# Kernel tuning notes

Hardware: AMD Instinct MI355X
Metric: run time of the kernel (lower is better)

The kernel has to match this reference:

```python
import jax, jax.numpy as jnp
import numpy as np

B, T, H, L = 64, 512, 768, 9


def _crf_logZ(logits, transitions, seqlen):
    # forward algorithm; state freezes at t >= seqlen (tfa semantics)
    Tn = logits.shape[1]
    alpha0 = logits[:, 0]  # [B,L]
    valid = (jnp.arange(1, Tn)[None, :] < seqlen[:, None]).T  # [T-1,B]
    xs = (jnp.swapaxes(logits[:, 1:], 0, 1), valid)

    def step(alpha, inp):
        logit_t, v = inp
        new = jax.nn.logsumexp(alpha[:, :, None] + transitions[None], axis=1) + logit_t
        return jnp.where(v[:, None], new, alpha), None

    alphaT, _ = jax.lax.scan(step, alpha0, xs)
    return jax.nn.logsumexp(alphaT, axis=1)  # [B]


def _crf_score(logits, transitions, label, seqlen):
    Tn = logits.shape[1]
    seqmask = (jnp.arange(Tn)[None, :] < seqlen[:, None]).astype(logits.dtype)  # [B,T]
    unary = jnp.take_along_axis(logits, label[..., None], axis=2)[..., 0]
    unary = jnp.sum(unary * seqmask, axis=1)
    trans = transitions[label[:, :-1], label[:, 1:]]
    trans = jnp.sum(trans * seqmask[:, 1:], axis=1)
    return unary + trans  # [B]


def _viterbi(logits, transitions, seqlen):
    Tn, Ln = logits.shape[1], logits.shape[2]
    alpha0 = logits[:, 0]
    valid = (jnp.arange(1, Tn)[None, :] < seqlen[:, None]).T  # [T-1,B]
    xs = (jnp.swapaxes(logits[:, 1:], 0, 1), valid)
    idL = jnp.arange(Ln, dtype=jnp.int32)

    def step(alpha, inp):
        logit_t, v = inp
        scores = alpha[:, :, None] + transitions[None]  # [B,L,L]
        new = jnp.max(scores, axis=1) + logit_t
        bp = jnp.argmax(scores, axis=1).astype(jnp.int32)  # [B,L]
        alpha = jnp.where(v[:, None], new, alpha)
        bp = jnp.where(v[:, None], bp, idL[None, :])  # identity bp on padded steps
        return alpha, bp

    alphaT, bps = jax.lax.scan(step, alpha0, xs)  # bps: [T-1,B,L]
    last = jnp.argmax(alphaT, axis=1).astype(jnp.int32)  # [B]

    def back(tag, bp):
        prev = jnp.take_along_axis(bp, tag[:, None], axis=1)[:, 0]
        return prev, tag

    first, rest = jax.lax.scan(back, last, bps, reverse=True)
    tags = jnp.concatenate([first[None], rest], axis=0)  # [T,B]
    return jnp.swapaxes(tags, 0, 1)  # [B,T]


def setup_inputs() -> dict:
    key = jax.random.key(0)
    k = jax.random.split(key, 6)
    x = jax.random.normal(k[0], (B, T, H), dtype=jnp.float32)
    W = jax.random.truncated_normal(k[1], -2.0, 2.0, (H, L), dtype=jnp.float32) * 0.02
    b = jnp.zeros((L,), dtype=jnp.float32)
    lim = float(np.sqrt(6.0 / (L + L)))  # glorot_uniform
    transitions = jax.random.uniform(k[2], (L, L), dtype=jnp.float32, minval=-lim, maxval=lim)
    label = jax.random.randint(k[3], (B, T), 0, L, dtype=jnp.int32)
    seqlen = jax.random.randint(k[4], (B,), 1, T + 1, dtype=jnp.int32)
    mask = jnp.arange(T)[None, :] < seqlen[:, None]
    return {"x": x, "W": W, "b": b, "transitions": transitions, "label": label, "seqlen": seqlen, "mask": mask}


def reference(x, W, b, transitions, label, seqlen, mask):
    logits = jnp.einsum('bth,hl->btl', x, W) + b  # dense_ner
    ll = _crf_score(logits, transitions, label, seqlen) - _crf_logZ(logits, transitions, seqlen)
    loss = jnp.mean(-ll)
    vit = _viterbi(logits, transitions, seqlen)
    seqmask = (jnp.arange(logits.shape[1])[None, :] < seqlen[:, None]).astype(jnp.float32)
    accuracy = jnp.sum((vit == label).astype(jnp.float32) * seqmask) / jnp.sum(seqlen.astype(jnp.float32))
    tp = jnp.sum(((label > 0) & (vit == label)).astype(jnp.float32))
    tn = jnp.sum(((label > 0) & (vit != label)).astype(jnp.float32))
    fp = jnp.sum((mask & (label == 0) & (vit > 0)).astype(jnp.float32))
    return vit, tp, tn, fp, loss, accuracy
```

## Files before the change

### kernel.cpp

```cpp
#include <hip/hip_runtime.h>
#include <stdint.h>
#include <math.h>

#define NB 64
#define BT 512
#define NH 768
#define NL 9
#define PBT 528
#define PADW 772

__device__ __forceinline__ float rlane(float v, int i) {
    return __int_as_float(__builtin_amdgcn_readlane(__float_as_int(v), i));
}

template<int CTRL, int RM>
__device__ __forceinline__ float dppadd(float v) {
    const int t = __builtin_amdgcn_update_dpp(0, __float_as_int(v), CTRL, RM, 0xf, true);
    return v + __int_as_float(t);
}

__device__ __forceinline__ float wave_sum_dpp(float v) {
    v = dppadd<0x111, 0xf>(v);
    v = dppadd<0x112, 0xf>(v);
    v = dppadd<0x114, 0xf>(v);
    v = dppadd<0x118, 0xf>(v);
    v = dppadd<0x142, 0xa>(v);
    v = dppadd<0x143, 0xc>(v);
    return rlane(v, 63);
}

__global__ __launch_bounds__(256, 2) void gemm_kernel(
    const float* __restrict__ x, const float* __restrict__ W,
    const float* __restrict__ bias, float* __restrict__ logits)
{
    __shared__ float wT[NL * PADW];

    const int tid  = threadIdx.x;
    const int lane = tid & 63;

    for (int i = tid; i < NH * NL; i += 256) {
        const int h = i / NL, l = i - h * NL;
        wT[l * PADW + h] = W[i];
    }
    __syncthreads();

    float wr[3][NL][4];
#pragma unroll
    for (int k = 0; k < 3; ++k)
#pragma unroll
        for (int l = 0; l < NL; ++l) {
            const float4 w4 = *(const float4*)&wT[l * PADW + k * 256 + lane * 4];
            wr[k][l][0] = w4.x; wr[k][l][1] = w4.y;
            wr[k][l][2] = w4.z; wr[k][l][3] = w4.w;
        }
    const float bj = bias[lane < NL ? lane : 0];

    const int gwave = (blockIdx.x * blockDim.x + tid) >> 6;
    const int nw    = (gridDim.x * blockDim.x) >> 6;
    const int nrows = NB * BT;
    int row = gwave;
    if (row >= nrows) return;

    const float4* xr = (const float4*)(x + (size_t)row * NH);
    float4 a0 = xr[lane], a1 = xr[64 + lane], a2 = xr[128 + lane];

    while (true) {
        const int nrow = row + nw;
        float4 b0, b1, b2;
        if (nrow < nrows) {
            const float4* xn = (const float4*)(x + (size_t)nrow * NH);
            b0 = xn[lane]; b1 = xn[64 + lane]; b2 = xn[128 + lane];
        }

        float acc[NL];
#pragma unroll
        for (int l = 0; l < NL; ++l) {
            float s = a0.x * wr[0][l][0];
            s = fmaf(a0.y, wr[0][l][1], s);
            s = fmaf(a0.z, wr[0][l][2], s);
            s = fmaf(a0.w, wr[0][l][3], s);
            s = fmaf(a1.x, wr[1][l][0], s);
            s = fmaf(a1.y, wr[1][l][1], s);
            s = fmaf(a1.z, wr[1][l][2], s);
            s = fmaf(a1.w, wr[1][l][3], s);
            s = fmaf(a2.x, wr[2][l][0], s);
            s = fmaf(a2.y, wr[2][l][1], s);
            s = fmaf(a2.z, wr[2][l][2], s);
            s = fmaf(a2.w, wr[2][l][3], s);
            acc[l] = s;
        }
        float sum[NL];
#pragma unroll
        for (int l = 0; l < NL; ++l) sum[l] = wave_sum_dpp(acc[l]);
        float outv = sum[0];
#pragma unroll
        for (int l = 1; l < NL; ++l) outv = (lane == l) ? sum[l] : outv;
        if (lane < NL) logits[(size_t)row * NL + lane] = outv + bj;

        row = nrow;
        if (row >= nrows) break;
        a0 = b0; a1 = b1; a2 = b2;
    }
}

__global__ __launch_bounds__(256) void crf_kernel(
    const float* __restrict__ logits, const float* __restrict__ trans,
    const int* __restrict__ label, const int* __restrict__ seqlen,
    float* __restrict__ vit_out, float* __restrict__ stats)
{
    __shared__ __align__(16) float lg_lds[PBT * NL];
    __shared__ float    val_lds[BT * NL];
    __shared__ float    trans_lds[NL * NL];
    __shared__ uint8_t  bp_lds[(BT - 1) * NL];
    __shared__ uint64_t packed_lds[BT - 1];
    __shared__ uint8_t  vit_lds[BT];
    __shared__ float    xw[4][4];

    const int b    = blockIdx.x;
    const int tid  = threadIdx.x;
    const int lane = tid & 63;
    const int wv   = tid >> 6;
    const int sl   = seqlen[b];
    const float* lg  = logits + (size_t)b * BT * NL;
    const int*   lab = label + (size_t)b * BT;

    {
        const float4* src = (const float4*)lg;
        float4* dst = (float4*)lg_lds;
        for (int idx = tid; idx < BT * NL / 4; idx += 256) dst[idx] = src[idx];
        for (int idx = BT * NL + tid; idx < PBT * NL; idx += 256) lg_lds[idx] = 0.f;
        if (tid < NL * NL) trans_lds[tid] = trans[tid];
    }
    __syncthreads();

    if (wv == 0) {
        const int j = lane < NL ? lane : 0;
        float E[NL];
#pragma unroll
        for (int i = 0; i < NL; ++i) E[i] = __expf(trans_lds[i * NL + j]) * 0.125f;
        float A = __expf(lg_lds[j]);
        int lc = 0;
        for (int tb = 1; tb < BT + 8; tb += 8) {
            float P[8];
#pragma unroll
            for (int s = 0; s < 8; ++s) P[s] = __expf(lg_lds[(tb + s) * NL + j]);
#pragma unroll
            for (int s = 0; s < 8; ++s) {
                const int t = tb + s;
                const float r0 = rlane(A, 0), r1 = rlane(A, 1), r2 = rlane(A, 2),
                            r3 = rlane(A, 3), r4 = rlane(A, 4), r5 = rlane(A, 5),
                            r6 = rlane(A, 6), r7 = rlane(A, 7), r8 = rlane(A, 8);
                float p0 = r0 * E[0]; p0 = fmaf(r1, E[1], p0); p0 = fmaf(r2, E[2], p0);
                float p1 = r3 * E[3]; p1 = fmaf(r4, E[4], p1); p1 = fmaf(r5, E[5], p1);
                float p2 = r6 * E[6]; p2 = fmaf(r7, E[7], p2); p2 = fmaf(r8, E[8], p2);
                const float An = ((p0 + p1) + p2) * P[s];
                A = (t < sl) ? An : A;
            }
            const float m = fmaxf(fmaxf(
                fmaxf(fmaxf(rlane(A, 0), rlane(A, 1)), fmaxf(rlane(A, 2), rlane(A, 3))),
                fmaxf(fmaxf(rlane(A, 4), rlane(A, 5)), fmaxf(rlane(A, 6), rlane(A, 7)))),
                rlane(A, 8));
            const int ex = (int)((__float_as_uint(m) >> 23) & 0xFFu) - 126;
            const float sc = __uint_as_float((uint32_t)(127 - ex) << 23);
            A *= sc;
            lc += ex;
        }
        const float sum = ((rlane(A, 0) + rlane(A, 1)) + (rlane(A, 2) + rlane(A, 3))) +
                          ((rlane(A, 4) + rlane(A, 5)) + (rlane(A, 6) + rlane(A, 7))) +
                          rlane(A, 8);
        const float logZ = logf(sum) +
            ((float)lc + 3.0f * (float)(sl - 1)) * 0.6931471805599453f;
        if (lane == 0) stats[b * 8 + 1] = logZ;
    } else if (wv == 1) {
        const int j = lane < NL ? lane : 0;
        float tc[NL];
#pragma unroll
        for (int i = 0; i < NL; ++i) tc[i] = trans_lds[i * NL + j];
        float v = lg_lds[j];
        if (lane < NL) val_lds[j] = v;
        for (int tb = 1; tb < BT + 8; tb += 8) {
            float lv[8];
#pragma unroll
            for (int s = 0; s < 8; ++s) lv[s] = lg_lds[(tb + s) * NL + j];
#pragma unroll
            for (int s = 0; s < 8; ++s) {
                const int t = tb + s;
                const float r0 = rlane(v, 0), r1 = rlane(v, 1), r2 = rlane(v, 2),
                            r3 = rlane(v, 3), r4 = rlane(v, 4), r5 = rlane(v, 5),
                            r6 = rlane(v, 6), r7 = rlane(v, 7), r8 = rlane(v, 8);
                const float c0 = r0 + tc[0], c1 = r1 + tc[1], c2 = r2 + tc[2],
                            c3 = r3 + tc[3], c4 = r4 + tc[4], c5 = r5 + tc[5],
                            c6 = r6 + tc[6], c7 = r7 + tc[7], c8 = r8 + tc[8];
                const float m = fmaxf(fmaxf(fmaxf(fmaxf(c0, c1), c2),
                                            fmaxf(fmaxf(c3, c4), c5)),
                                      fmaxf(fmaxf(c6, c7), c8));
                const float nv = m + lv[s];
                v = (t < sl) ? nv : v;
                if (lane < NL && t < BT) val_lds[t * NL + lane] = v;
            }
        }
        const float r0 = rlane(v, 0), r1 = rlane(v, 1), r2 = rlane(v, 2),
                    r3 = rlane(v, 3), r4 = rlane(v, 4), r5 = rlane(v, 5),
                    r6 = rlane(v, 6), r7 = rlane(v, 7), r8 = rlane(v, 8);
        const float m = fmaxf(fmaxf(fmaxf(fmaxf(r0, r1), r2),
                                    fmaxf(fmaxf(r3, r4), r5)),
                              fmaxf(fmaxf(r6, r7), r8));
        const int last = (r0 == m) ? 0 : (r1 == m) ? 1 : (r2 == m) ? 2 :
                         (r3 == m) ? 3 : (r4 == m) ? 4 : (r5 == m) ? 5 :
                         (r6 == m) ? 6 : (r7 == m) ? 7 : 8;
        if (lane == 0) vit_lds[BT - 1] = (uint8_t)last;
    } else if (wv == 2) {
        float s = 0.f;
        for (int t = lane; t < BT; t += 64) {
            const int lb = lab[t];
            if (t < sl) {
                s += lg_lds[t * NL + lb];
                if (t >= 1) s += trans_lds[lab[t - 1] * NL + lb];
            }
        }
#pragma unroll
        for (int off = 32; off >= 1; off >>= 1) s += __shfl_xor(s, off, 64);
        if (lane == 0) stats[b * 8 + 0] = s;
    }
    __syncthreads();

    for (int idx = tid; idx < (BT - 1) * NL; idx += 256) {
        const int tm1 = idx / NL;
        const int jj  = idx - tm1 * NL;
        const int t   = tm1 + 1;
        int bi;
        if (t >= sl) bi = jj;
        else {
            float best = val_lds[tm1 * NL] + trans_lds[jj];
            bi = 0;
#pragma unroll
            for (int i = 1; i < NL; ++i) {
                const float c = val_lds[tm1 * NL + i] + trans_lds[i * NL + jj];
                if (c > best) { best = c; bi = i; }
            }
        }
        bp_lds[idx] = (uint8_t)bi;
    }
    __syncthreads();

    for (int r = tid; r < BT - 1; r += 256) {
        uint64_t p = 0;
#pragma unroll
        for (int i = 0; i < NL; ++i)
            p |= (uint64_t)bp_lds[r * NL + i] << (4 * i);
        packed_lds[r] = p;
    }
    __syncthreads();

    if (tid == 0) {
        int tag = vit_lds[BT - 1];
        for (int t = BT - 2; t >= 0; --t) {
            const uint64_t row = packed_lds[t];
            tag = (int)((row >> (4 * tag)) & 15u);
            vit_lds[t] = (uint8_t)tag;
        }
    }
    __syncthreads();

    float accv = 0.f, tpv = 0.f, tnv = 0.f, fpv = 0.f;
    for (int t = tid; t < BT; t += 256) {
        const int tg = vit_lds[t];
        const int lb = lab[t];
        const bool msk = t < sl;
        vit_out[(size_t)b * BT + t] = (float)tg;
        if (msk && tg == lb) accv += 1.f;
        if (lb > 0 && tg == lb) tpv += 1.f;
        if (lb > 0 && tg != lb) tnv += 1.f;
        if (msk && lb == 0 && tg > 0) fpv += 1.f;
    }
#pragma unroll
    for (int off = 32; off >= 1; off >>= 1) {
        accv += __shfl_xor(accv, off, 64);
        tpv  += __shfl_xor(tpv,  off, 64);
        tnv  += __shfl_xor(tnv,  off, 64);
        fpv  += __shfl_xor(fpv,  off, 64);
    }
    if (lane == 0) { xw[0][wv] = accv; xw[1][wv] = tpv; xw[2][wv] = tnv; xw[3][wv] = fpv; }
    __syncthreads();
    if (tid == 0) {
        stats[b * 8 + 2] = xw[0][0] + xw[0][1] + xw[0][2] + xw[0][3];
        stats[b * 8 + 3] = xw[1][0] + xw[1][1] + xw[1][2] + xw[1][3];
        stats[b * 8 + 4] = xw[2][0] + xw[2][1] + xw[2][2] + xw[2][3];
        stats[b * 8 + 5] = xw[3][0] + xw[3][1] + xw[3][2] + xw[3][3];
    }
}

__global__ __launch_bounds__(64) void finalize_kernel(
    const float* __restrict__ stats, const int* __restrict__ seqlen,
    float* __restrict__ out)
{
    const int lane = threadIdx.x;
    float score = stats[lane * 8 + 0];
    float logZ  = stats[lane * 8 + 1];
    float accv  = stats[lane * 8 + 2];
    float tpv   = stats[lane * 8 + 3];
    float tnv   = stats[lane * 8 + 4];
    float fpv   = stats[lane * 8 + 5];
    float nll   = logZ - score;
    float slf   = (float)seqlen[lane];
#pragma unroll
    for (int off = 32; off >= 1; off >>= 1) {
        nll  += __shfl_xor(nll,  off, 64);
        accv += __shfl_xor(accv, off, 64);
        tpv  += __shfl_xor(tpv,  off, 64);
        tnv  += __shfl_xor(tnv,  off, 64);
        fpv  += __shfl_xor(fpv,  off, 64);
        slf  += __shfl_xor(slf,  off, 64);
    }
    if (lane == 0) {
        out[NB * BT + 0] = tpv;
        out[NB * BT + 1] = tnv;
        out[NB * BT + 2] = fpv;
        out[NB * BT + 3] = nll / (float)NB;
        out[NB * BT + 4] = accv / slf;
    }
}

extern "C" void kernel_launch(void* const* d_in, const int* in_sizes, int n_in,
                              void* d_out, int out_size, void* d_ws, size_t ws_size,
                              hipStream_t stream)
{
    const float* x      = (const float*)d_in[0];
    const float* W      = (const float*)d_in[1];
    const float* bias   = (const float*)d_in[2];
    const float* trans  = (const float*)d_in[3];
    const int*   label  = (const int*)d_in[4];
    const int*   seqlen = (const int*)d_in[5];

    float* out    = (float*)d_out;
    float* logits = (float*)d_ws;
    float* stats  = logits + (size_t)NB * BT * NL;

    gemm_kernel<<<512, 256, 0, stream>>>(x, W, bias, logits);
    crf_kernel<<<NB, 256, 0, stream>>>(logits, trans, label, seqlen, out, stats);
    finalize_kernel<<<1, 64, 0, stream>>>(stats, seqlen, out);
}
```

Measured before the change: 212.7 us.

## Pack four CRF sequences per wave and compute backpointers inline in Viterbi scan

The CRF kernel now handles four batch rows per block, with lanes 0-35 of one wave each owning one (sequence, label) pair. Neighbour values are gathered with ds_bpermute instead of readlane. Logits are read directly from global memory with one-block-ahead register prefetching instead of being staged in LDS. Viterbi backpointers are computed inside the forward scan, which removes the separate val_lds pass. The block count drops from 64 to 16, so the serial scans run four sequences per wave, trading the lower latency of readlane for fewer, longer-lived blocks and less total serial work.

```diff
diff --git a/kernel.cpp b/kernel.cpp
--- a/kernel.cpp
+++ b/kernel.cpp
@@ -6,11 +6,15 @@
 #define BT 512
 #define NH 768
 #define NL 9
-#define PBT 528
 #define PADW 772
+#define CBB 4
+#define BPROW 16
 
 __device__ __forceinline__ float rlane(float v, int i) {
     return __int_as_float(__builtin_amdgcn_readlane(__float_as_int(v), i));
+}
+__device__ __forceinline__ float bperm(int addr, float v) {
+    return __int_as_float(__builtin_amdgcn_ds_bpermute(addr, __float_as_int(v)));
 }
 
 template<int CTRL, int RM>
@@ -18,7 +22,6 @@
     const int t = __builtin_amdgcn_update_dpp(0, __float_as_int(v), CTRL, RM, 0xf, true);
     return v + __int_as_float(t);
 }
-
 __device__ __forceinline__ float wave_sum_dpp(float v) {
     v = dppadd<0x111, 0xf>(v);
     v = dppadd<0x112, 0xf>(v);
@@ -108,185 +111,222 @@
     const int* __restrict__ label, const int* __restrict__ seqlen,
     float* __restrict__ vit_out, float* __restrict__ stats)
 {
-    __shared__ __align__(16) float lg_lds[PBT * NL];
-    __shared__ float    val_lds[BT * NL];
     __shared__ float    trans_lds[NL * NL];
-    __shared__ uint8_t  bp_lds[(BT - 1) * NL];
-    __shared__ uint64_t packed_lds[BT - 1];
-    __shared__ uint8_t  vit_lds[BT];
+    __shared__ uint8_t  bp_lds[CBB][(BT - 1) * BPROW];
+    __shared__ uint64_t packed_lds[CBB][BT - 1];
+    __shared__ uint8_t  vit_lds[CBB][BT];
     __shared__ float    xw[4][4];
 
-    const int b    = blockIdx.x;
     const int tid  = threadIdx.x;
     const int lane = tid & 63;
     const int wv   = tid >> 6;
-    const int sl   = seqlen[b];
-    const float* lg  = logits + (size_t)b * BT * NL;
-    const int*   lab = label + (size_t)b * BT;
-
-    {
-        const float4* src = (const float4*)lg;
-        float4* dst = (float4*)lg_lds;
-        for (int idx = tid; idx < BT * NL / 4; idx += 256) dst[idx] = src[idx];
-        for (int idx = BT * NL + tid; idx < PBT * NL; idx += 256) lg_lds[idx] = 0.f;
-        if (tid < NL * NL) trans_lds[tid] = trans[tid];
-    }
-    __syncthreads();
+    const int b0   = blockIdx.x * CBB;
+
+    if (tid < NL * NL) trans_lds[tid] = trans[tid];
+    __syncthreads();
+
+    int bl = lane / 9, j = lane - bl * 9;
+    if (lane >= 36) { bl = 3; j = 8; }
+    const bool act = (lane < 36);
+    const int bg   = b0 + bl;
+    const int sl   = seqlen[bg];
+    const float* lgb = logits + (size_t)bg * BT * NL;
+    int adr[9];
+#pragma unroll
+    for (int i = 0; i < 9; ++i) adr[i] = (bl * 9 + i) * 4;
 
     if (wv == 0) {
-        const int j = lane < NL ? lane : 0;
-        float E[NL];
-#pragma unroll
-        for (int i = 0; i < NL; ++i) E[i] = __expf(trans_lds[i * NL + j]) * 0.125f;
-        float A = __expf(lg_lds[j]);
+        float E[9];
+#pragma unroll
+        for (int i = 0; i < 9; ++i) E[i] = __expf(trans_lds[i * NL + j]) * 0.125f;
+        float A = __expf(lgb[j]);
         int lc = 0;
+        float cur[8], nxt[8];
+#pragma unroll
+        for (int s = 0; s < 8; ++s) cur[s] = lgb[(1 + s) * NL + j];
         for (int tb = 1; tb < BT + 8; tb += 8) {
+#pragma unroll
+            for (int s = 0; s < 8; ++s) {
+                int tt = tb + 8 + s; tt = tt > BT - 1 ? BT - 1 : tt;
+                nxt[s] = lgb[tt * NL + j];
+            }
             float P[8];
 #pragma unroll
-            for (int s = 0; s < 8; ++s) P[s] = __expf(lg_lds[(tb + s) * NL + j]);
+            for (int s = 0; s < 8; ++s) P[s] = __expf(cur[s]);
 #pragma unroll
             for (int s = 0; s < 8; ++s) {
                 const int t = tb + s;
-                const float r0 = rlane(A, 0), r1 = rlane(A, 1), r2 = rlane(A, 2),
-                            r3 = rlane(A, 3), r4 = rlane(A, 4), r5 = rlane(A, 5),
-                            r6 = rlane(A, 6), r7 = rlane(A, 7), r8 = rlane(A, 8);
-                float p0 = r0 * E[0]; p0 = fmaf(r1, E[1], p0); p0 = fmaf(r2, E[2], p0);
-                float p1 = r3 * E[3]; p1 = fmaf(r4, E[4], p1); p1 = fmaf(r5, E[5], p1);
-                float p2 = r6 * E[6]; p2 = fmaf(r7, E[7], p2); p2 = fmaf(r8, E[8], p2);
+                const float g0 = bperm(adr[0], A), g1 = bperm(adr[1], A),
+                            g2 = bperm(adr[2], A), g3 = bperm(adr[3], A),
+                            g4 = bperm(adr[4], A), g5 = bperm(adr[5], A),
+                            g6 = bperm(adr[6], A), g7 = bperm(adr[7], A),
+                            g8 = bperm(adr[8], A);
+                float p0 = g0 * E[0]; p0 = fmaf(g1, E[1], p0); p0 = fmaf(g2, E[2], p0);
+                float p1 = g3 * E[3]; p1 = fmaf(g4, E[4], p1); p1 = fmaf(g5, E[5], p1);
+                float p2 = g6 * E[6]; p2 = fmaf(g7, E[7], p2); p2 = fmaf(g8, E[8], p2);
                 const float An = ((p0 + p1) + p2) * P[s];
                 A = (t < sl) ? An : A;
             }
-            const float m = fmaxf(fmaxf(
-                fmaxf(fmaxf(rlane(A, 0), rlane(A, 1)), fmaxf(rlane(A, 2), rlane(A, 3))),
-                fmaxf(fmaxf(rlane(A, 4), rlane(A, 5)), fmaxf(rlane(A, 6), rlane(A, 7)))),
-                rlane(A, 8));
-            const int ex = (int)((__float_as_uint(m) >> 23) & 0xFFu) - 126;
-            const float sc = __uint_as_float((uint32_t)(127 - ex) << 23);
-            A *= sc;
-            lc += ex;
-        }
-        const float sum = ((rlane(A, 0) + rlane(A, 1)) + (rlane(A, 2) + rlane(A, 3))) +
-                          ((rlane(A, 4) + rlane(A, 5)) + (rlane(A, 6) + rlane(A, 7))) +
-                          rlane(A, 8);
+            {
+                const float g0 = bperm(adr[0], A), g1 = bperm(adr[1], A),
+                            g2 = bperm(adr[2], A), g3 = bperm(adr[3], A),
+                            g4 = bperm(adr[4], A), g5 = bperm(adr[5], A),
+                            g6 = bperm(adr[6], A), g7 = bperm(adr[7], A),
+                            g8 = bperm(adr[8], A);
+                const float m = fmaxf(fmaxf(
+                    fmaxf(fmaxf(g0, g1), fmaxf(g2, g3)),
+                    fmaxf(fmaxf(g4, g5), fmaxf(g6, g7))), g8);
+                const int ex = (int)((__float_as_uint(m) >> 23) & 0xFFu) - 126;
+                const float sc = __uint_as_float((uint32_t)(127 - ex) << 23);
+                A *= sc;
+                lc += ex;
+            }
+#pragma unroll
+            for (int s = 0; s < 8; ++s) cur[s] = nxt[s];
+        }
+        const float g0 = bperm(adr[0], A), g1 = bperm(adr[1], A),
+                    g2 = bperm(adr[2], A), g3 = bperm(adr[3], A),
+                    g4 = bperm(adr[4], A), g5 = bperm(adr[5], A),
+                    g6 = bperm(adr[6], A), g7 = bperm(adr[7], A),
+                    g8 = bperm(adr[8], A);
+        const float sum = ((g0 + g1) + (g2 + g3)) + ((g4 + g5) + (g6 + g7)) + g8;
         const float logZ = logf(sum) +
             ((float)lc + 3.0f * (float)(sl - 1)) * 0.6931471805599453f;
-        if (lane == 0) stats[b * 8 + 1] = logZ;
+        if (act && j == 0) stats[bg * 8 + 1] = logZ;
     } else if (wv == 1) {
-        const int j = lane < NL ? lane : 0;
-        float tc[NL];
-#pragma unroll
-        for (int i = 0; i < NL; ++i) tc[i] = trans_lds[i * NL + j];
-        float v = lg_lds[j];
-        if (lane < NL) val_lds[j] = v;
+        float tc[9];
+#pragma unroll
+        for (int i = 0; i < 9; ++i) tc[i] = trans_lds[i * NL + j];
+        float v = lgb[j];
+        float cur[8], nxt[8];
+#pragma unroll
+        for (int s = 0; s < 8; ++s) cur[s] = lgb[(1 + s) * NL + j];
         for (int tb = 1; tb < BT + 8; tb += 8) {
-            float lv[8];
-#pragma unroll
-            for (int s = 0; s < 8; ++s) lv[s] = lg_lds[(tb + s) * NL + j];
+#pragma unroll
+            for (int s = 0; s < 8; ++s) {
+                int tt = tb + 8 + s; tt = tt > BT - 1 ? BT - 1 : tt;
+                nxt[s] = lgb[tt * NL + j];
+            }
 #pragma unroll
             for (int s = 0; s < 8; ++s) {
                 const int t = tb + s;
-                const float r0 = rlane(v, 0), r1 = rlane(v, 1), r2 = rlane(v, 2),
-                            r3 = rlane(v, 3), r4 = rlane(v, 4), r5 = rlane(v, 5),
-                            r6 = rlane(v, 6), r7 = rlane(v, 7), r8 = rlane(v, 8);
-                const float c0 = r0 + tc[0], c1 = r1 + tc[1], c2 = r2 + tc[2],
-                            c3 = r3 + tc[3], c4 = r4 + tc[4], c5 = r5 + tc[5],
-                            c6 = r6 + tc[6], c7 = r7 + tc[7], c8 = r8 + tc[8];
+                const float g0 = bperm(adr[0], v), g1 = bperm(adr[1], v),
+                            g2 = bperm(adr[2], v), g3 = bperm(adr[3], v),
+                            g4 = bperm(adr[4], v), g5 = bperm(adr[5], v),
+                            g6 = bperm(adr[6], v), g7 = bperm(adr[7], v),
+                            g8 = bperm(adr[8], v);
+                const float c0 = g0 + tc[0], c1 = g1 + tc[1], c2 = g2 + tc[2],
+                            c3 = g3 + tc[3], c4 = g4 + tc[4], c5 = g5 + tc[5],
+                            c6 = g6 + tc[6], c7 = g7 + tc[7], c8 = g8 + tc[8];
                 const float m = fmaxf(fmaxf(fmaxf(fmaxf(c0, c1), c2),
                                             fmaxf(fmaxf(c3, c4), c5)),
                                       fmaxf(fmaxf(c6, c7), c8));
-                const float nv = m + lv[s];
+                const float nv = m + cur[s];
                 v = (t < sl) ? nv : v;
-                if (lane < NL && t < BT) val_lds[t * NL + lane] = v;
-            }
-        }
-        const float r0 = rlane(v, 0), r1 = rlane(v, 1), r2 = rlane(v, 2),
-                    r3 = rlane(v, 3), r4 = rlane(v, 4), r5 = rlane(v, 5),
-                    r6 = rlane(v, 6), r7 = rlane(v, 7), r8 = rlane(v, 8);
-        const float m = fmaxf(fmaxf(fmaxf(fmaxf(r0, r1), r2),
-                                    fmaxf(fmaxf(r3, r4), r5)),
-                              fmaxf(fmaxf(r6, r7), r8));
-        const int last = (r0 == m) ? 0 : (r1 == m) ? 1 : (r2 == m) ? 2 :
-                         (r3 == m) ? 3 : (r4 == m) ? 4 : (r5 == m) ? 5 :
-                         (r6 == m) ? 6 : (r7 == m) ? 7 : 8;
-        if (lane == 0) vit_lds[BT - 1] = (uint8_t)last;
-    } else if (wv == 2) {
-        float s = 0.f;
-        for (int t = lane; t < BT; t += 64) {
+                int bi = 8;
+                bi = (c7 == m) ? 7 : bi;
+                bi = (c6 == m) ? 6 : bi;
+                bi = (c5 == m) ? 5 : bi;
+                bi = (c4 == m) ? 4 : bi;
+                bi = (c3 == m) ? 3 : bi;
+                bi = (c2 == m) ? 2 : bi;
+                bi = (c1 == m) ? 1 : bi;
+                bi = (c0 == m) ? 0 : bi;
+                bi = (t < sl) ? bi : j;
+                if (act && t < BT)
+                    bp_lds[bl][(t - 1) * BPROW + j] = (uint8_t)bi;
+            }
+#pragma unroll
+            for (int s = 0; s < 8; ++s) cur[s] = nxt[s];
+        }
+        const float g0 = bperm(adr[0], v), g1 = bperm(adr[1], v),
+                    g2 = bperm(adr[2], v), g3 = bperm(adr[3], v),
+                    g4 = bperm(adr[4], v), g5 = bperm(adr[5], v),
+                    g6 = bperm(adr[6], v), g7 = bperm(adr[7], v),
+                    g8 = bperm(adr[8], v);
+        const float m = fmaxf(fmaxf(fmaxf(fmaxf(g0, g1), g2),
+                                    fmaxf(fmaxf(g3, g4), g5)),
+                              fmaxf(fmaxf(g6, g7), g8));
+        const int last = (g0 == m) ? 0 : (g1 == m) ? 1 : (g2 == m) ? 2 :
+                         (g3 == m) ? 3 : (g4 == m) ? 4 : (g5 == m) ? 5 :
+                         (g6 == m) ? 6 : (g7 == m) ? 7 : 8;
+        if (act && j == 0) vit_lds[bl][BT - 1] = (uint8_t)last;
+    } else {
+        const int s0 = (wv - 2) * 2;
+#pragma unroll
+        for (int k = 0; k < 2; ++k) {
+            const int bb  = s0 + k;
+            const int bgs = b0 + bb;
+            const int sls = seqlen[bgs];
+            const int* lab = label + (size_t)bgs * BT;
+            const float* lgs = logits + (size_t)bgs * BT * NL;
+            float s = 0.f;
+            for (int t = lane; t < BT; t += 64) {
+                const int lb = lab[t];
+                if (t < sls) {
+                    s += lgs[t * NL + lb];
+                    if (t >= 1) s += trans_lds[lab[t - 1] * NL + lb];
+                }
+            }
+#pragma unroll
+            for (int off = 32; off >= 1; off >>= 1) s += __shfl_xor(s, off, 64);
+            if (lane == 0) stats[bgs * 8 + 0] = s;
+        }
+    }
+    __syncthreads();
+
+    for (int idx = tid; idx < CBB * (BT - 1); idx += 256) {
+        const int bb = idx / (BT - 1);
+        const int rr = idx - bb * (BT - 1);
+        uint64_t p = 0;
+#pragma unroll
+        for (int i = 0; i < NL; ++i)
+            p |= (uint64_t)bp_lds[bb][rr * BPROW + i] << (4 * i);
+        packed_lds[bb][rr] = p;
+    }
+    __syncthreads();
+
+    if (wv == 0 && lane < CBB) {
+        int tag = vit_lds[lane][BT - 1];
+        for (int t = BT - 2; t >= 0; --t) {
+            const uint64_t row = packed_lds[lane][t];
+            tag = (int)((row >> (4 * tag)) & 15u);
+            vit_lds[lane][t] = (uint8_t)tag;
+        }
+    }
+    __syncthreads();
+
+    for (int bb = 0; bb < CBB; ++bb) {
+        const int b   = b0 + bb;
+        const int sls = seqlen[b];
+        const int* lab = label + (size_t)b * BT;
+        float accv = 0.f, tpv = 0.f, tnv = 0.f, fpv = 0.f;
+        for (int t = tid; t < BT; t += 256) {
+            const int tg = vit_lds[bb][t];
             const int lb = lab[t];
-            if (t < sl) {
-                s += lg_lds[t * NL + lb];
-                if (t >= 1) s += trans_lds[lab[t - 1] * NL + lb];
-            }
-        }
-#pragma unroll
-        for (int off = 32; off >= 1; off >>= 1) s += __shfl_xor(s, off, 64);
-        if (lane == 0) stats[b * 8 + 0] = s;
-    }
-    __syncthreads();
-
-    for (int idx = tid; idx < (BT - 1) * NL; idx += 256) {
-        const int tm1 = idx / NL;
-        const int jj  = idx - tm1 * NL;
-        const int t   = tm1 + 1;
-        int bi;
-        if (t >= sl) bi = jj;
-        else {
-            float best = val_lds[tm1 * NL] + trans_lds[jj];
-            bi = 0;
-#pragma unroll
-            for (int i = 1; i < NL; ++i) {
-                const float c = val_lds[tm1 * NL + i] + trans_lds[i * NL + jj];
-                if (c > best) { best = c; bi = i; }
-            }
-        }
-        bp_lds[idx] = (uint8_t)bi;
-    }
-    __syncthreads();
-
-    for (int r = tid; r < BT - 1; r += 256) {
-        uint64_t p = 0;
-#pragma unroll
-        for (int i = 0; i < NL; ++i)
-            p |= (uint64_t)bp_lds[r * NL + i] << (4 * i);
-        packed_lds[r] = p;
-    }
-    __syncthreads();
-
-    if (tid == 0) {
-        int tag = vit_lds[BT - 1];
-        for (int t = BT - 2; t >= 0; --t) {
-            const uint64_t row = packed_lds[t];
-            tag = (int)((row >> (4 * tag)) & 15u);
-            vit_lds[t] = (uint8_t)tag;
-        }
-    }
-    __syncthreads();
-
-    float accv = 0.f, tpv = 0.f, tnv = 0.f, fpv = 0.f;
-    for (int t = tid; t < BT; t += 256) {
-        const int tg = vit_lds[t];
-        const int lb = lab[t];
-        const bool msk = t < sl;
-        vit_out[(size_t)b * BT + t] = (float)tg;
-        if (msk && tg == lb) accv += 1.f;
-        if (lb > 0 && tg == lb) tpv += 1.f;
-        if (lb > 0 && tg != lb) tnv += 1.f;
-        if (msk && lb == 0 && tg > 0) fpv += 1.f;
-    }
-#pragma unroll
-    for (int off = 32; off >= 1; off >>= 1) {
-        accv += __shfl_xor(accv, off, 64);
-        tpv  += __shfl_xor(tpv,  off, 64);
-        tnv  += __shfl_xor(tnv,  off, 64);
-        fpv  += __shfl_xor(fpv,  off, 64);
-    }
-    if (lane == 0) { xw[0][wv] = accv; xw[1][wv] = tpv; xw[2][wv] = tnv; xw[3][wv] = fpv; }
-    __syncthreads();
-    if (tid == 0) {
-        stats[b * 8 + 2] = xw[0][0] + xw[0][1] + xw[0][2] + xw[0][3];
-        stats[b * 8 + 3] = xw[1][0] + xw[1][1] + xw[1][2] + xw[1][3];
-        stats[b * 8 + 4] = xw[2][0] + xw[2][1] + xw[2][2] + xw[2][3];
-        stats[b * 8 + 5] = xw[3][0] + xw[3][1] + xw[3][2] + xw[3][3];
+            const bool msk = t < sls;
+            vit_out[(size_t)b * BT + t] = (float)tg;
+            if (msk && tg == lb) accv += 1.f;
+            if (lb > 0 && tg == lb) tpv += 1.f;
+            if (lb > 0 && tg != lb) tnv += 1.f;
+            if (msk && lb == 0 && tg > 0) fpv += 1.f;
+        }
+#pragma unroll
+        for (int off = 32; off >= 1; off >>= 1) {
+            accv += __shfl_xor(accv, off, 64);
+            tpv  += __shfl_xor(tpv,  off, 64);
+            tnv  += __shfl_xor(tnv,  off, 64);
+            fpv  += __shfl_xor(fpv,  off, 64);
+        }
+        if (lane == 0) { xw[0][wv] = accv; xw[1][wv] = tpv; xw[2][wv] = tnv; xw[3][wv] = fpv; }
+        __syncthreads();
+        if (tid == 0) {
+            stats[b * 8 + 2] = xw[0][0] + xw[0][1] + xw[0][2] + xw[0][3];
+            stats[b * 8 + 3] = xw[1][0] + xw[1][1] + xw[1][2] + xw[1][3];
+            stats[b * 8 + 4] = xw[2][0] + xw[2][1] + xw[2][2] + xw[2][3];
+            stats[b * 8 + 5] = xw[3][0] + xw[3][1] + xw[3][2] + xw[3][3];
+        }
+        __syncthreads();
     }
 }
 
@@ -337,6 +377,6 @@
     float* stats  = logits + (size_t)NB * BT * NL;
 
     gemm_kernel<<<512, 256, 0, stream>>>(x, W, bias, logits);
-    crf_kernel<<<NB, 256, 0, stream>>>(logits, trans, label, seqlen, out, stats);
+    crf_kernel<<<NB / CBB, 256, 0, stream>>>(logits, trans, label, seqlen, out, stats);
     finalize_kernel<<<1, 64, 0, stream>>>(stats, seqlen, out);
 }
```

New measurement: 273.9 us. 28.8% more time.

## Use DPP row shifts instead of readlane in CRF recurrences, fuse backpointer packing

Applied to the files above, without the earlier changes.

The forward (logZ) and Viterbi recurrences now gather neighbouring lanes' state with DPP row_shr/row_shl moves, with per-lane transition coefficients indexed by shift distance, instead of nine scalar readlane broadcasts per step. Out-of-range shifts are neutralised with zero or -1e30 coefficients. The aim is to remove the readlane-to-SGPR round trip from the serial per-timestep dependency chain. Backpointer computation is also merged with packing: each thread handles one timestep and writes the packed 64-bit row directly, which drops a byte LDS array and a barrier. The backtrace loop is unrolled. In exchange each step issues 16 DPP moves instead of 9 readlanes, and the code relies on the 9 labels sitting in lanes 0-8 of a single DPP row.

```diff
diff --git a/kernel.cpp b/kernel.cpp
--- a/kernel.cpp
+++ b/kernel.cpp
@@ -13,12 +13,17 @@
     return __int_as_float(__builtin_amdgcn_readlane(__float_as_int(v), i));
 }
 
+template<int CTRL>
+__device__ __forceinline__ float dmov(float v) {
+    return __int_as_float(__builtin_amdgcn_update_dpp(
+        0, __float_as_int(v), CTRL, 0xf, 0xf, true));
+}
+
 template<int CTRL, int RM>
 __device__ __forceinline__ float dppadd(float v) {
     const int t = __builtin_amdgcn_update_dpp(0, __float_as_int(v), CTRL, RM, 0xf, true);
     return v + __int_as_float(t);
 }
-
 __device__ __forceinline__ float wave_sum_dpp(float v) {
     v = dppadd<0x111, 0xf>(v);
     v = dppadd<0x112, 0xf>(v);
@@ -111,7 +116,6 @@
     __shared__ __align__(16) float lg_lds[PBT * NL];
     __shared__ float    val_lds[BT * NL];
     __shared__ float    trans_lds[NL * NL];
-    __shared__ uint8_t  bp_lds[(BT - 1) * NL];
     __shared__ uint64_t packed_lds[BT - 1];
     __shared__ uint8_t  vit_lds[BT];
     __shared__ float    xw[4][4];
@@ -133,11 +137,17 @@
     }
     __syncthreads();
 
+    const int j = lane < NL ? lane : 0;
+
     if (wv == 0) {
-        const int j = lane < NL ? lane : 0;
-        float E[NL];
-#pragma unroll
-        for (int i = 0; i < NL; ++i) E[i] = __expf(trans_lds[i * NL + j]) * 0.125f;
+        const float Eo = __expf(trans_lds[j * NL + j]) * 0.125f;
+        float Cs[8], Ds[8], Ms[8];
+#pragma unroll
+        for (int k = 1; k <= 8; ++k) {
+            Cs[k - 1] = (j >= k)     ? __expf(trans_lds[(j - k) * NL + j]) * 0.125f : 0.f;
+            Ds[k - 1] = (j + k <= 8) ? __expf(trans_lds[(j + k) * NL + j]) * 0.125f : 0.f;
+            Ms[k - 1] = (j + k <= 8) ? 1.f : 0.f;
+        }
         float A = __expf(lg_lds[j]);
         int lc = 0;
         for (int tb = 1; tb < BT + 8; tb += 8) {
@@ -147,35 +157,73 @@
 #pragma unroll
             for (int s = 0; s < 8; ++s) {
                 const int t = tb + s;
-                const float r0 = rlane(A, 0), r1 = rlane(A, 1), r2 = rlane(A, 2),
-                            r3 = rlane(A, 3), r4 = rlane(A, 4), r5 = rlane(A, 5),
-                            r6 = rlane(A, 6), r7 = rlane(A, 7), r8 = rlane(A, 8);
-                float p0 = r0 * E[0]; p0 = fmaf(r1, E[1], p0); p0 = fmaf(r2, E[2], p0);
-                float p1 = r3 * E[3]; p1 = fmaf(r4, E[4], p1); p1 = fmaf(r5, E[5], p1);
-                float p2 = r6 * E[6]; p2 = fmaf(r7, E[7], p2); p2 = fmaf(r8, E[8], p2);
-                const float An = ((p0 + p1) + p2) * P[s];
+                const float g1 = dmov<0x111>(A), g2 = dmov<0x112>(A),
+                            g3 = dmov<0x113>(A), g4 = dmov<0x114>(A),
+                            g5 = dmov<0x115>(A), g6 = dmov<0x116>(A),
+                            g7 = dmov<0x117>(A), g8 = dmov<0x118>(A);
+                const float h1 = dmov<0x101>(A), h2 = dmov<0x102>(A),
+                            h3 = dmov<0x103>(A), h4 = dmov<0x104>(A),
+                            h5 = dmov<0x105>(A), h6 = dmov<0x106>(A),
+                            h7 = dmov<0x107>(A), h8 = dmov<0x108>(A);
+                float s0 = A * Eo;
+                s0 = fmaf(g1, Cs[0], s0); s0 = fmaf(g2, Cs[1], s0);
+                s0 = fmaf(g3, Cs[2], s0); s0 = fmaf(g4, Cs[3], s0);
+                float s1 = g5 * Cs[4];
+                s1 = fmaf(g6, Cs[5], s1); s1 = fmaf(g7, Cs[6], s1);
+                s1 = fmaf(g8, Cs[7], s1);
+                float s2 = h1 * Ds[0];
+                s2 = fmaf(h2, Ds[1], s2); s2 = fmaf(h3, Ds[2], s2);
+                s2 = fmaf(h4, Ds[3], s2);
+                float s3 = h5 * Ds[4];
+                s3 = fmaf(h6, Ds[5], s3); s3 = fmaf(h7, Ds[6], s3);
+                s3 = fmaf(h8, Ds[7], s3);
+                const float An = ((s0 + s1) + (s2 + s3)) * P[s];
                 A = (t < sl) ? An : A;
             }
-            const float m = fmaxf(fmaxf(
-                fmaxf(fmaxf(rlane(A, 0), rlane(A, 1)), fmaxf(rlane(A, 2), rlane(A, 3))),
-                fmaxf(fmaxf(rlane(A, 4), rlane(A, 5)), fmaxf(rlane(A, 6), rlane(A, 7)))),
-                rlane(A, 8));
-            const int ex = (int)((__float_as_uint(m) >> 23) & 0xFFu) - 126;
-            const float sc = __uint_as_float((uint32_t)(127 - ex) << 23);
-            A *= sc;
-            lc += ex;
-        }
-        const float sum = ((rlane(A, 0) + rlane(A, 1)) + (rlane(A, 2) + rlane(A, 3))) +
-                          ((rlane(A, 4) + rlane(A, 5)) + (rlane(A, 6) + rlane(A, 7))) +
-                          rlane(A, 8);
-        const float logZ = logf(sum) +
-            ((float)lc + 3.0f * (float)(sl - 1)) * 0.6931471805599453f;
-        if (lane == 0) stats[b * 8 + 1] = logZ;
+            {
+                const float g1 = dmov<0x111>(A), g2 = dmov<0x112>(A),
+                            g3 = dmov<0x113>(A), g4 = dmov<0x114>(A),
+                            g5 = dmov<0x115>(A), g6 = dmov<0x116>(A),
+                            g7 = dmov<0x117>(A), g8 = dmov<0x118>(A);
+                const float h1 = dmov<0x101>(A), h2 = dmov<0x102>(A),
+                            h3 = dmov<0x103>(A), h4 = dmov<0x104>(A),
+                            h5 = dmov<0x105>(A), h6 = dmov<0x106>(A),
+                            h7 = dmov<0x107>(A), h8 = dmov<0x108>(A);
+                float m = A;
+                m = fmaxf(m, fmaxf(fmaxf(g1, g2), fmaxf(g3, g4)));
+                m = fmaxf(m, fmaxf(fmaxf(g5, g6), fmaxf(g7, g8)));
+                m = fmaxf(m, fmaxf(fmaxf(h1 * Ms[0], h2 * Ms[1]),
+                                   fmaxf(h3 * Ms[2], h4 * Ms[3])));
+                m = fmaxf(m, fmaxf(fmaxf(h5 * Ms[4], h6 * Ms[5]),
+                                   fmaxf(h7 * Ms[6], h8 * Ms[7])));
+                const int ex = (int)((__float_as_uint(m) >> 23) & 0xFFu) - 126;
+                const float sc = __uint_as_float((uint32_t)(127 - ex) << 23);
+                A *= sc;
+                lc += ex;
+            }
+        }
+        {
+            const float h1 = dmov<0x101>(A), h2 = dmov<0x102>(A),
+                        h3 = dmov<0x103>(A), h4 = dmov<0x104>(A),
+                        h5 = dmov<0x105>(A), h6 = dmov<0x106>(A),
+                        h7 = dmov<0x107>(A), h8 = dmov<0x108>(A);
+            float u = A;
+            u = fmaf(h1, Ms[0], u); u = fmaf(h2, Ms[1], u);
+            u = fmaf(h3, Ms[2], u); u = fmaf(h4, Ms[3], u);
+            u = fmaf(h5, Ms[4], u); u = fmaf(h6, Ms[5], u);
+            u = fmaf(h7, Ms[6], u); u = fmaf(h8, Ms[7], u);
+            const float logZ = logf(u) +
+                ((float)lc + 3.0f * (float)(sl - 1)) * 0.6931471805599453f;
+            if (lane == 0) stats[b * 8 + 1] = logZ;
+        }
     } else if (wv == 1) {
-        const int j = lane < NL ? lane : 0;
-        float tc[NL];
-#pragma unroll
-        for (int i = 0; i < NL; ++i) tc[i] = trans_lds[i * NL + j];
+        const float To = trans_lds[j * NL + j];
+        float Ts[8], Us[8];
+#pragma unroll
+        for (int k = 1; k <= 8; ++k) {
+            Ts[k - 1] = (j >= k)     ? trans_lds[(j - k) * NL + j] : -1e30f;
+            Us[k - 1] = (j + k <= 8) ? trans_lds[(j + k) * NL + j] : -1e30f;
+        }
         float v = lg_lds[j];
         if (lane < NL) val_lds[j] = v;
         for (int tb = 1; tb < BT + 8; tb += 8) {
@@ -185,15 +233,26 @@
 #pragma unroll
             for (int s = 0; s < 8; ++s) {
                 const int t = tb + s;
-                const float r0 = rlane(v, 0), r1 = rlane(v, 1), r2 = rlane(v, 2),
-                            r3 = rlane(v, 3), r4 = rlane(v, 4), r5 = rlane(v, 5),
-                            r6 = rlane(v, 6), r7 = rlane(v, 7), r8 = rlane(v, 8);
-                const float c0 = r0 + tc[0], c1 = r1 + tc[1], c2 = r2 + tc[2],
-                            c3 = r3 + tc[3], c4 = r4 + tc[4], c5 = r5 + tc[5],
-                            c6 = r6 + tc[6], c7 = r7 + tc[7], c8 = r8 + tc[8];
-                const float m = fmaxf(fmaxf(fmaxf(fmaxf(c0, c1), c2),
-                                            fmaxf(fmaxf(c3, c4), c5)),
-                                      fmaxf(fmaxf(c6, c7), c8));
+                const float g1 = dmov<0x111>(v), g2 = dmov<0x112>(v),
+                            g3 = dmov<0x113>(v), g4 = dmov<0x114>(v),
+                            g5 = dmov<0x115>(v), g6 = dmov<0x116>(v),
+                            g7 = dmov<0x117>(v), g8 = dmov<0x118>(v);
+                const float h1 = dmov<0x101>(v), h2 = dmov<0x102>(v),
+                            h3 = dmov<0x103>(v), h4 = dmov<0x104>(v),
+                            h5 = dmov<0x105>(v), h6 = dmov<0x106>(v),
+                            h7 = dmov<0x107>(v), h8 = dmov<0x108>(v);
+                const float c0 = v + To;
+                const float c1 = g1 + Ts[0], c2 = g2 + Ts[1], c3 = g3 + Ts[2],
+                            c4 = g4 + Ts[3], c5 = g5 + Ts[4], c6 = g6 + Ts[5],
+                            c7 = g7 + Ts[6], c8 = g8 + Ts[7];
+                const float d1 = h1 + Us[0], d2 = h2 + Us[1], d3 = h3 + Us[2],
+                            d4 = h4 + Us[3], d5 = h5 + Us[4], d6 = h6 + Us[5],
+                            d7 = h7 + Us[6], d8 = h8 + Us[7];
+                const float m = fmaxf(
+                    fmaxf(fmaxf(fmaxf(c0, c1), c2), fmaxf(fmaxf(c3, c4), c5)),
+                    fmaxf(fmaxf(fmaxf(c6, c7), c8), fmaxf(
+                        fmaxf(fmaxf(d1, d2), fmaxf(d3, d4)),
+                        fmaxf(fmaxf(d5, d6), fmaxf(d7, d8)))));
                 const float nv = m + lv[s];
                 v = (t < sl) ? nv : v;
                 if (lane < NL && t < BT) val_lds[t * NL + lane] = v;
@@ -224,36 +283,35 @@
     }
     __syncthreads();
 
-    for (int idx = tid; idx < (BT - 1) * NL; idx += 256) {
-        const int tm1 = idx / NL;
-        const int jj  = idx - tm1 * NL;
-        const int t   = tm1 + 1;
-        int bi;
-        if (t >= sl) bi = jj;
-        else {
-            float best = val_lds[tm1 * NL] + trans_lds[jj];
-            bi = 0;
-#pragma unroll
-            for (int i = 1; i < NL; ++i) {
-                const float c = val_lds[tm1 * NL + i] + trans_lds[i * NL + jj];
-                if (c > best) { best = c; bi = i; }
+    for (int tm1 = tid; tm1 < BT - 1; tm1 += 256) {
+        const int t = tm1 + 1;
+        uint64_t p;
+        if (t >= sl) {
+            p = 0x876543210ull;
+        } else {
+            float vv[NL];
+#pragma unroll
+            for (int i = 0; i < NL; ++i) vv[i] = val_lds[tm1 * NL + i];
+            p = 0;
+#pragma unroll
+            for (int jj = 0; jj < NL; ++jj) {
+                float best = vv[0] + trans_lds[jj];
+                int bi = 0;
+#pragma unroll
+                for (int i = 1; i < NL; ++i) {
+                    const float c = vv[i] + trans_lds[i * NL + jj];
+                    if (c > best) { best = c; bi = i; }
+                }
+                p |= (uint64_t)bi << (4 * jj);
             }
         }
-        bp_lds[idx] = (uint8_t)bi;
-    }
-    __syncthreads();
-
-    for (int r = tid; r < BT - 1; r += 256) {
-        uint64_t p = 0;
-#pragma unroll
-        for (int i = 0; i < NL; ++i)
-            p |= (uint64_t)bp_lds[r * NL + i] << (4 * i);
-        packed_lds[r] = p;
+        packed_lds[tm1] = p;
     }
     __syncthreads();
 
     if (tid == 0) {
         int tag = vit_lds[BT - 1];
+#pragma unroll 8
         for (int t = BT - 2; t >= 0; --t) {
             const uint64_t row = packed_lds[t];
             tag = (int)((row >> (4 * tag)) & 15u);
```

After: 220.6 us. 1.04x slower.
